# Optimization experiments

Measured on AMD Instinct MI355X. Metric: run time of the kernel, lower is better.

The kernel has to match this reference:

```python
import jax, jax.numpy as jnp
import numpy as np

N = 4096
D = 512   # d_model == dff (required by the original code path)
H = 4
NEG = -1e10
ALPHA = 0.3  # keras LeakyReLU default alpha


def setup_inputs() -> dict:
    key = jax.random.key(0)
    ks = jax.random.split(key, 8)
    nodes = jax.random.normal(ks[0], (N, D), dtype=jnp.float32)
    # sparse-ish 0/1 dense adjacency with self loops
    adj = (jax.random.uniform(ks[1], (N, N)) < 0.01).astype(jnp.float32)
    adj = jnp.maximum(adj, jnp.eye(N, dtype=jnp.float32))
    s = 0.05
    W_node = jax.random.normal(ks[2], (D, D), dtype=jnp.float32) * s
    b_node = jnp.zeros((D,), dtype=jnp.float32)
    K = jax.random.normal(ks[3], (H, D, D), dtype=jnp.float32) * s
    A_self = jax.random.normal(ks[4], (H, D), dtype=jnp.float32) * s
    A_neigh = jax.random.normal(ks[5], (H, D), dtype=jnp.float32) * s
    return {"nodes": nodes, "adj": adj, "W_node": W_node, "b_node": b_node,
            "K": K, "A_self": A_self, "A_neigh": A_neigh, "num_heads": H}


def reference(nodes, adj, W_node, b_node, K, A_self, A_neigh, num_heads):
    # node_layer: Dense(dff)
    x = nodes @ W_node + b_node                       # [N, D]
    # per-head projection, vectorized over heads
    feats = jnp.einsum('nd,hdf->hnf', x, K)           # [H, N, D]
    # additive attention scores; both terms are per-row scalars -> [H, N]
    s = jnp.einsum('hnf,hf->hn', feats, A_self) + jnp.einsum('hnf,hf->hn', feats, A_neigh)
    s = jnp.where(s > 0, s, ALPHA * s)                # LeakyReLU(alpha=0.3)
    # broadcast row score over columns + adjacency mask, softmax over neighbors
    logits = s[:, :, None] + NEG * (1.0 - adj)[None]  # [H, N, N]
    attn = jax.nn.softmax(logits, axis=-1)
    # dropout is identity at inference (training=False)
    out = jnp.einsum('hij,hjf->hif', attn, feats)     # [H, N, D]
    out = jnp.mean(out, axis=0)                       # mean over heads
    return jax.nn.relu(out)
```

## Files before the change

### kernel.cpp

```cpp
#include <hip/hip_runtime.h>


typedef short  short8 __attribute__((ext_vector_type(8)));
typedef float  f32x4  __attribute__((ext_vector_type(4)));

__device__ inline unsigned short f2bf(float f) {
    union { float f; unsigned int u; } v; v.f = f;
    unsigned int u = v.u;
    u += 0x7fffu + ((u >> 16) & 1u);
    return (unsigned short)(u >> 16);
}

__global__ __launch_bounds__(256) void kbarT_kernel(
        const float* __restrict__ K, unsigned short* __restrict__ KbarT,
        int D, int H, float invH) {
    __shared__ float tile[64][65];
    const int f0 = blockIdx.x * 64, d0 = blockIdx.y * 64;
    const int tid = threadIdx.x;
    const int c4 = (tid & 15) * 4;
    const int DD = D * D;

    for (int rr = tid >> 4; rr < 64; rr += 16) {
        float sx = 0.f, sy = 0.f, sz = 0.f, sw = 0.f;
        for (int h = 0; h < H; ++h) {
            float4 v = *reinterpret_cast<const float4*>(
                &K[(size_t)h * DD + (size_t)(d0 + rr) * D + f0 + c4]);
            sx += v.x; sy += v.y; sz += v.z; sw += v.w;
        }
        tile[rr][c4 + 0] = sx * invH;
        tile[rr][c4 + 1] = sy * invH;
        tile[rr][c4 + 2] = sz * invH;
        tile[rr][c4 + 3] = sw * invH;
    }
    __syncthreads();
    for (int fr = tid >> 4; fr < 64; fr += 16) {
        ushort4 o;
        o.x = f2bf(tile[c4 + 0][fr]);
        o.y = f2bf(tile[c4 + 1][fr]);
        o.z = f2bf(tile[c4 + 2][fr]);
        o.w = f2bf(tile[c4 + 3][fr]);
        *reinterpret_cast<ushort4*>(&KbarT[(size_t)(f0 + fr) * D + d0 + c4]) = o;
    }
}

template <bool CA, bool CB>
__device__ inline void gemm_body(const void* __restrict__ Ap,
                                 const void* __restrict__ Btp,
                                 const float* __restrict__ bias,
                                 unsigned short* __restrict__ C,
                                 int Nn, int K, int bx, int by) {
    __shared__ unsigned short As[64][32];
    __shared__ unsigned short Bs[64][32];
    const int tid  = threadIdx.x;
    const int lane = tid & 63;
    const int wave = tid >> 6;
    const int wy = wave >> 1, wx = wave & 1;
    const int row0 = by * 64, col0 = bx * 64;
    const int l15 = lane & 15, quad = lane >> 4;
    const int ldr = tid >> 2;
    const int ldk = (tid & 3) * 8;

    f32x4 acc[2][2] = {};

    for (int k0 = 0; k0 < K; k0 += 32) {
        short8 av, bv;
        if (CA) {
            const float* a = (const float*)Ap + (size_t)(row0 + ldr) * K + k0 + ldk;
            float4 x = *reinterpret_cast<const float4*>(a);
            float4 y = *reinterpret_cast<const float4*>(a + 4);
            av[0] = (short)f2bf(x.x); av[1] = (short)f2bf(x.y);
            av[2] = (short)f2bf(x.z); av[3] = (short)f2bf(x.w);
            av[4] = (short)f2bf(y.x); av[5] = (short)f2bf(y.y);
            av[6] = (short)f2bf(y.z); av[7] = (short)f2bf(y.w);
        } else {
            av = *reinterpret_cast<const short8*>(
                (const unsigned short*)Ap + (size_t)(row0 + ldr) * K + k0 + ldk);
        }
        if (CB) {
            const float* b = (const float*)Btp + (size_t)(col0 + ldr) * K + k0 + ldk;
            float4 x = *reinterpret_cast<const float4*>(b);
            float4 y = *reinterpret_cast<const float4*>(b + 4);
            bv[0] = (short)f2bf(x.x); bv[1] = (short)f2bf(x.y);
            bv[2] = (short)f2bf(x.z); bv[3] = (short)f2bf(x.w);
            bv[4] = (short)f2bf(y.x); bv[5] = (short)f2bf(y.y);
            bv[6] = (short)f2bf(y.z); bv[7] = (short)f2bf(y.w);
        } else {
            bv = *reinterpret_cast<const short8*>(
                (const unsigned short*)Btp + (size_t)(col0 + ldr) * K + k0 + ldk);
        }
        __syncthreads();
        *reinterpret_cast<short8*>(&As[ldr][ldk]) = av;
        *reinterpret_cast<short8*>(&Bs[ldr][ldk]) = bv;
        __syncthreads();
        short8 a0 = *reinterpret_cast<const short8*>(&As[wy * 32 +      l15][quad * 8]);
        short8 a1 = *reinterpret_cast<const short8*>(&As[wy * 32 + 16 + l15][quad * 8]);
        short8 b0 = *reinterpret_cast<const short8*>(&Bs[wx * 32 +      l15][quad * 8]);
        short8 b1 = *reinterpret_cast<const short8*>(&Bs[wx * 32 + 16 + l15][quad * 8]);
        acc[0][0] = __builtin_amdgcn_mfma_f32_16x16x32_bf16(a0, b0, acc[0][0], 0, 0, 0);
        acc[0][1] = __builtin_amdgcn_mfma_f32_16x16x32_bf16(a0, b1, acc[0][1], 0, 0, 0);
        acc[1][0] = __builtin_amdgcn_mfma_f32_16x16x32_bf16(a1, b0, acc[1][0], 0, 0, 0);
        acc[1][1] = __builtin_amdgcn_mfma_f32_16x16x32_bf16(a1, b1, acc[1][1], 0, 0, 0);
    }

#pragma unroll
    for (int mi = 0; mi < 2; ++mi)
#pragma unroll
        for (int ni = 0; ni < 2; ++ni) {
            int col = col0 + wx * 32 + ni * 16 + l15;
            float bvl = bias ? bias[col] : 0.f;
#pragma unroll
            for (int r = 0; r < 4; ++r) {
                int row = row0 + wy * 32 + mi * 16 + quad * 4 + r;
                C[(size_t)row * Nn + col] = f2bf(acc[mi][ni][r] + bvl);
            }
        }
}

__global__ __launch_bounds__(256) void gemm1_kernel(
        const unsigned short* __restrict__ KbarT, const float* __restrict__ W,
        const float* __restrict__ b, unsigned short* __restrict__ MmatT,
        float* __restrict__ bias2, int D, int gemmY) {
    if ((int)blockIdx.y >= gemmY) {
        int e = ((int)blockIdx.y - gemmY) * gridDim.x + blockIdx.x;
        int wave = threadIdx.x >> 6, lane = threadIdx.x & 63;
        int f = e * 4 + wave;
        if (f >= D) return;
        const unsigned short* kr = KbarT + (size_t)f * D + lane * 8;
        const float* br = b + lane * 8;
        float s = 0.f;
#pragma unroll
        for (int j = 0; j < 8; ++j) {
            union { unsigned int i; float f; } v; v.i = ((unsigned int)kr[j]) << 16;
            s += br[j] * v.f;
        }
#pragma unroll
        for (int off = 32; off; off >>= 1) s += __shfl_down(s, off, 64);
        if (lane == 0) bias2[f] = s;
        return;
    }
    gemm_body<false, true>(KbarT, W, nullptr, MmatT, D, D, blockIdx.x, blockIdx.y);
}

__global__ __launch_bounds__(256) void gemm2_kernel(
        const float* __restrict__ nodes, const unsigned short* __restrict__ MmatT,
        const float* __restrict__ bias2, unsigned short* __restrict__ g,
        int D, int K) {
    gemm_body<true, false>(nodes, MmatT, bias2, g, D, K, blockIdx.x, blockIdx.y);
}

__global__ __launch_bounds__(256) void aggregate_kernel(
        const float* __restrict__ adj, const unsigned short* __restrict__ g,
        float* __restrict__ out, int N, int D) {
    const int row = blockIdx.x;
    const int tid = threadIdx.x;
    __shared__ int lst[1024];
    __shared__ int cnt;
    if (tid == 0) cnt = 0;
    __syncthreads();

    const float* arow = adj + (size_t)row * N;
    const int nper = N >> 8;
    const int base = tid * nper;
    const float4* ap = reinterpret_cast<const float4*>(arow + base);
    for (int c = 0; c < (nper >> 2); ++c) {
        float4 a = ap[c];
        int b4 = base + c * 4;
        if (a.x > 0.5f) { int p = atomicAdd(&cnt, 1); if (p < 1024) lst[p] = b4;     }
        if (a.y > 0.5f) { int p = atomicAdd(&cnt, 1); if (p < 1024) lst[p] = b4 + 1; }
        if (a.z > 0.5f) { int p = atomicAdd(&cnt, 1); if (p < 1024) lst[p] = b4 + 2; }
        if (a.w > 0.5f) { int p = atomicAdd(&cnt, 1); if (p < 1024) lst[p] = b4 + 3; }
    }
    __syncthreads();
    int deg = cnt; if (deg > 1024) deg = 1024;

    const int col = tid * 2;
    float acc0 = 0.f, acc1 = 0.f;
    int k = 0;
    for (; k + 8 <= deg; k += 8) {
        unsigned int u[8];
#pragma unroll
        for (int j = 0; j < 8; ++j)
            u[j] = *reinterpret_cast<const unsigned int*>(&g[(size_t)lst[k + j] * D + col]);
#pragma unroll
        for (int j = 0; j < 8; ++j) {
            union { unsigned int i; float f; } lo, hi;
            lo.i = u[j] << 16; hi.i = u[j] & 0xffff0000u;
            acc0 += lo.f; acc1 += hi.f;
        }
    }
    for (; k < deg; ++k) {
        unsigned int u = *reinterpret_cast<const unsigned int*>(&g[(size_t)lst[k] * D + col]);
        union { unsigned int i; float f; } lo, hi;
        lo.i = u << 16; hi.i = u & 0xffff0000u;
        acc0 += lo.f; acc1 += hi.f;
    }

    float inv = deg > 0 ? 1.f / (float)deg : 0.f;
    acc0 *= inv; acc1 *= inv;
    float2 o;
    o.x = acc0 > 0.f ? acc0 : 0.f;
    o.y = acc1 > 0.f ? acc1 : 0.f;
    *reinterpret_cast<float2*>(&out[(size_t)row * D + col]) = o;
}

extern "C" void kernel_launch(void* const* d_in, const int* in_sizes, int n_in,
                              void* d_out, int out_size, void* d_ws, size_t ws_size,
                              hipStream_t stream) {
    const float* nodes  = (const float*)d_in[0];
    const float* adj    = (const float*)d_in[1];
    const float* W_node = (const float*)d_in[2];
    const float* b_node = (const float*)d_in[3];
    const float* K      = (const float*)d_in[4];

    const int D  = in_sizes[3];
    const int N  = in_sizes[0] / D;
    const int H  = in_sizes[4] / (D * D);
    const int DD = D * D;

    float* out = (float*)d_out;

    char* ws = (char*)d_ws;
    unsigned short* KbarT  = (unsigned short*)(ws);
    unsigned short* MmatT  = (unsigned short*)(ws + (size_t)DD * 2);
    unsigned short* g_bf16 = (unsigned short*)(ws + (size_t)DD * 4);
    float*          bias2  = (float*)        (ws + (size_t)DD * 4 + (size_t)N * D * 2);

    {
        dim3 grid(D / 64, D / 64);
        kbarT_kernel<<<grid, 256, 0, stream>>>(K, KbarT, D, H, 1.0f / (float)H);
    }

    {
        int gx = D / 64, gemmY = D / 64;
        int biasRows = (D / 4 + gx - 1) / gx;
        dim3 grid(gx, gemmY + biasRows);
        gemm1_kernel<<<grid, 256, 0, stream>>>(KbarT, W_node, b_node, MmatT, bias2, D, gemmY);
    }

    {
        dim3 grid(D / 64, N / 64);
        gemm2_kernel<<<grid, 256, 0, stream>>>(nodes, MmatT, bias2, g_bf16, D, D);
    }

    aggregate_kernel<<<N, 256, 0, stream>>>(adj, g_bf16, out, N, D);
}
```

Baseline: 159.9 us.

## Widen aggregate kernel to 1024 threads with split-neighbor partial sums

The aggregation kernel now runs 1024 threads per row. Each thread reads one float4 of the adjacency row with a nontemporal load, and four thread groups each accumulate a strided quarter of the neighbor list. The partial sums are reduced through shared memory, and the output is written with a nontemporal store. The aim is more memory-level parallelism on the adjacency scan and the gathers from g. In exchange it adds an extra barrier and a shared-memory reduction, and it hardcodes N=4096 and D=512.

```diff
diff --git a/kernel.cpp b/kernel.cpp
--- a/kernel.cpp
+++ b/kernel.cpp
@@ -3,6 +3,8 @@
 
 typedef short  short8 __attribute__((ext_vector_type(8)));
 typedef float  f32x4  __attribute__((ext_vector_type(4)));
+typedef float  fv4    __attribute__((ext_vector_type(4)));
+typedef float  fv2    __attribute__((ext_vector_type(2)));
 
 __device__ inline unsigned short f2bf(float f) {
     union { float f; unsigned int u; } v; v.f = f;
@@ -148,23 +150,21 @@
     gemm_body<true, false>(nodes, MmatT, bias2, g, D, K, blockIdx.x, blockIdx.y);
 }
 
-__global__ __launch_bounds__(256) void aggregate_kernel(
+__global__ __launch_bounds__(1024) void aggregate_kernel(
         const float* __restrict__ adj, const unsigned short* __restrict__ g,
         float* __restrict__ out, int N, int D) {
     const int row = blockIdx.x;
     const int tid = threadIdx.x;
     __shared__ int lst[1024];
     __shared__ int cnt;
+    __shared__ float part[4][512];
     if (tid == 0) cnt = 0;
     __syncthreads();
 
-    const float* arow = adj + (size_t)row * N;
-    const int nper = N >> 8;
-    const int base = tid * nper;
-    const float4* ap = reinterpret_cast<const float4*>(arow + base);
-    for (int c = 0; c < (nper >> 2); ++c) {
-        float4 a = ap[c];
-        int b4 = base + c * 4;
+    {
+        const fv4* ap = reinterpret_cast<const fv4*>(adj + (size_t)row * N);
+        fv4 a = __builtin_nontemporal_load(ap + tid);
+        int b4 = tid * 4;
         if (a.x > 0.5f) { int p = atomicAdd(&cnt, 1); if (p < 1024) lst[p] = b4;     }
         if (a.y > 0.5f) { int p = atomicAdd(&cnt, 1); if (p < 1024) lst[p] = b4 + 1; }
         if (a.z > 0.5f) { int p = atomicAdd(&cnt, 1); if (p < 1024) lst[p] = b4 + 2; }
@@ -173,34 +173,43 @@
     __syncthreads();
     int deg = cnt; if (deg > 1024) deg = 1024;
 
-    const int col = tid * 2;
+    const int grp = tid >> 8;
+    const int sub = tid & 255;
+    const int col = sub * 2;
     float acc0 = 0.f, acc1 = 0.f;
-    int k = 0;
-    for (; k + 8 <= deg; k += 8) {
-        unsigned int u[8];
-#pragma unroll
-        for (int j = 0; j < 8; ++j)
-            u[j] = *reinterpret_cast<const unsigned int*>(&g[(size_t)lst[k + j] * D + col]);
-#pragma unroll
-        for (int j = 0; j < 8; ++j) {
-            union { unsigned int i; float f; } lo, hi;
-            lo.i = u[j] << 16; hi.i = u[j] & 0xffff0000u;
-            acc0 += lo.f; acc1 += hi.f;
-        }
-    }
-    for (; k < deg; ++k) {
+    int k = grp;
+    for (; k + 12 < deg; k += 16) {
+        unsigned int u0 = *reinterpret_cast<const unsigned int*>(&g[(size_t)lst[k     ] * D + col]);
+        unsigned int u1 = *reinterpret_cast<const unsigned int*>(&g[(size_t)lst[k +  4] * D + col]);
+        unsigned int u2 = *reinterpret_cast<const unsigned int*>(&g[(size_t)lst[k +  8] * D + col]);
+        unsigned int u3 = *reinterpret_cast<const unsigned int*>(&g[(size_t)lst[k + 12] * D + col]);
+        union { unsigned int i; float f; } lo, hi;
+        lo.i = u0 << 16; hi.i = u0 & 0xffff0000u; acc0 += lo.f; acc1 += hi.f;
+        lo.i = u1 << 16; hi.i = u1 & 0xffff0000u; acc0 += lo.f; acc1 += hi.f;
+        lo.i = u2 << 16; hi.i = u2 & 0xffff0000u; acc0 += lo.f; acc1 += hi.f;
+        lo.i = u3 << 16; hi.i = u3 & 0xffff0000u; acc0 += lo.f; acc1 += hi.f;
+    }
+    for (; k < deg; k += 4) {
         unsigned int u = *reinterpret_cast<const unsigned int*>(&g[(size_t)lst[k] * D + col]);
         union { unsigned int i; float f; } lo, hi;
         lo.i = u << 16; hi.i = u & 0xffff0000u;
         acc0 += lo.f; acc1 += hi.f;
     }
-
-    float inv = deg > 0 ? 1.f / (float)deg : 0.f;
-    acc0 *= inv; acc1 *= inv;
-    float2 o;
-    o.x = acc0 > 0.f ? acc0 : 0.f;
-    o.y = acc1 > 0.f ? acc1 : 0.f;
-    *reinterpret_cast<float2*>(&out[(size_t)row * D + col]) = o;
+    part[grp][col]     = acc0;
+    part[grp][col + 1] = acc1;
+    __syncthreads();
+
+    if (tid < 256) {
+        int c = tid * 2;
+        float s0 = part[0][c] + part[1][c] + part[2][c] + part[3][c];
+        float s1 = part[0][c + 1] + part[1][c + 1] + part[2][c + 1] + part[3][c + 1];
+        float inv = deg > 0 ? 1.f / (float)deg : 0.f;
+        s0 *= inv; s1 *= inv;
+        fv2 o;
+        o.x = s0 > 0.f ? s0 : 0.f;
+        o.y = s1 > 0.f ? s1 : 0.f;
+        __builtin_nontemporal_store(o, reinterpret_cast<fv2*>(&out[(size_t)row * D + c]));
+    }
 }
 
 extern "C" void kernel_launch(void* const* d_in, const int* in_sizes, int n_in,
@@ -242,5 +251,5 @@
         gemm2_kernel<<<grid, 256, 0, stream>>>(nodes, MmatT, bias2, g_bf16, D, D);
     }
 
-    aggregate_kernel<<<N, 256, 0, stream>>>(adj, g_bf16, out, N, D);
-}
+    aggregate_kernel<<<N, 1024, 0, stream>>>(adj, g_bf16, out, N, D);
+}
```

Result: slower. 167.8 us (+4.9%).

## Split adjacency scan into a grid-wide kernel separate from neighbor gather

Applied to the files above, without the earlier changes.

Moves the adjacency-to-neighbor-list compaction out of the per-row aggregate kernel into a standalone scan kernel that spreads the 64 MB adjacency read over many blocks, writing neighbor indices and counts to the workspace via global atomics. A separate gather kernel then loads each row's list into shared memory and sums bf16 features. The goal is to improve bandwidth utilization on the dominant adjacency read. The cost is an extra memset, an extra launch, global atomic contention per row, and a nonzero test on the raw float bits instead of a > 0.5 comparison.

```diff
diff --git a/kernel.cpp b/kernel.cpp
--- a/kernel.cpp
+++ b/kernel.cpp
@@ -148,30 +148,32 @@
     gemm_body<true, false>(nodes, MmatT, bias2, g, D, K, blockIdx.x, blockIdx.y);
 }
 
-__global__ __launch_bounds__(256) void aggregate_kernel(
-        const float* __restrict__ adj, const unsigned short* __restrict__ g,
-        float* __restrict__ out, int N, int D) {
+__global__ __launch_bounds__(256) void scan_kernel(
+        const unsigned int* __restrict__ adj_u, int* __restrict__ nbr,
+        int* __restrict__ cnt, int N) {
+    int idx = blockIdx.x * 256 + threadIdx.x;
+    int q = N >> 2;
+    int row = idx / q;
+    int base = (idx - row * q) * 4;
+    const uint4 a = reinterpret_cast<const uint4*>(adj_u)[idx];
+    int* nrow = nbr + (size_t)row * 1024;
+    if (a.x) { int p = atomicAdd(&cnt[row], 1); if (p < 1024) nrow[p] = base;     }
+    if (a.y) { int p = atomicAdd(&cnt[row], 1); if (p < 1024) nrow[p] = base + 1; }
+    if (a.z) { int p = atomicAdd(&cnt[row], 1); if (p < 1024) nrow[p] = base + 2; }
+    if (a.w) { int p = atomicAdd(&cnt[row], 1); if (p < 1024) nrow[p] = base + 3; }
+}
+
+__global__ __launch_bounds__(256) void gather_kernel(
+        const int* __restrict__ nbr, const int* __restrict__ cnt,
+        const unsigned short* __restrict__ g, float* __restrict__ out,
+        int N, int D) {
     const int row = blockIdx.x;
     const int tid = threadIdx.x;
     __shared__ int lst[1024];
-    __shared__ int cnt;
-    if (tid == 0) cnt = 0;
+    int deg = cnt[row]; if (deg > 1024) deg = 1024;
+    const int* nrow = nbr + (size_t)row * 1024;
+    for (int k = tid; k < deg; k += 256) lst[k] = nrow[k];
     __syncthreads();
-
-    const float* arow = adj + (size_t)row * N;
-    const int nper = N >> 8;
-    const int base = tid * nper;
-    const float4* ap = reinterpret_cast<const float4*>(arow + base);
-    for (int c = 0; c < (nper >> 2); ++c) {
-        float4 a = ap[c];
-        int b4 = base + c * 4;
-        if (a.x > 0.5f) { int p = atomicAdd(&cnt, 1); if (p < 1024) lst[p] = b4;     }
-        if (a.y > 0.5f) { int p = atomicAdd(&cnt, 1); if (p < 1024) lst[p] = b4 + 1; }
-        if (a.z > 0.5f) { int p = atomicAdd(&cnt, 1); if (p < 1024) lst[p] = b4 + 2; }
-        if (a.w > 0.5f) { int p = atomicAdd(&cnt, 1); if (p < 1024) lst[p] = b4 + 3; }
-    }
-    __syncthreads();
-    int deg = cnt; if (deg > 1024) deg = 1024;
 
     const int col = tid * 2;
     float acc0 = 0.f, acc1 = 0.f;
@@ -224,6 +226,10 @@
     unsigned short* MmatT  = (unsigned short*)(ws + (size_t)DD * 2);
     unsigned short* g_bf16 = (unsigned short*)(ws + (size_t)DD * 4);
     float*          bias2  = (float*)        (ws + (size_t)DD * 4 + (size_t)N * D * 2);
+    int*            cnt    = (int*)          (ws + (size_t)DD * 4 + (size_t)N * D * 2 + (size_t)D * 4);
+    int*            nbr    = (int*)          (ws + (size_t)DD * 4 + (size_t)N * D * 2 + (size_t)D * 4 + (size_t)N * 4);
+
+    hipMemsetAsync(cnt, 0, (size_t)N * 4, stream);
 
     {
         dim3 grid(D / 64, D / 64);
@@ -237,10 +243,13 @@
         gemm1_kernel<<<grid, 256, 0, stream>>>(KbarT, W_node, b_node, MmatT, bias2, D, gemmY);
     }
 
+    scan_kernel<<<(N / 4) * (N / 256), 256, 0, stream>>>(
+        (const unsigned int*)adj, nbr, cnt, N);
+
     {
         dim3 grid(D / 64, N / 64);
         gemm2_kernel<<<grid, 256, 0, stream>>>(nodes, MmatT, bias2, g_bf16, D, D);
     }
 
-    aggregate_kernel<<<N, 256, 0, stream>>>(adj, g_bf16, out, N, D);
-}
+    gather_kernel<<<N, 256, 0, stream>>>(nbr, cnt, g_bf16, out, N, D);
+}
```

Result: slower. 216.6 us (+35.5%).
